# Kernel tuning notes

Hardware: AMD Instinct MI355X
Metric: run time of the kernel (lower is better)

The kernel has to match this reference:

```python
import jax, jax.numpy as jnp
import numpy as np

B, C, D = 8192, 1000, 2048
CLAMP_MIN, CLAMP_MAX = 1e-12, 1e12
SEP_WEIGHT = 0.001


def setup_inputs() -> dict:
    key = jax.random.key(0)
    k1, k2, k3 = jax.random.split(key, 3)
    x = jax.random.normal(k1, (B, D), dtype=jnp.float32)
    centers = jax.random.normal(k2, (C, D), dtype=jnp.float32)
    labels = jax.random.randint(k3, (B,), 0, C, dtype=jnp.int64)
    return {"x": x, "centers": centers, "labels": labels}


def reference(x, centers, labels):
    distmat = (
        jnp.sum(x * x, axis=1, keepdims=True)
        + jnp.sum(centers * centers, axis=1)[None, :]
        - 2.0 * (x @ centers.T)
    )
    d = jnp.clip(distmat, CLAMP_MIN, CLAMP_MAX)
    mask = labels[:, None] == jnp.arange(C, dtype=labels.dtype)[None, :]  # [B, C]
    bsz = x.shape[0]
    ncls = centers.shape[0]
    # each row has exactly one True in mask -> counts are B and B*(C-1)
    center_loss = jnp.sum(jnp.where(mask, d, 0.0)) / bsz
    sep_loss = jnp.sum(jnp.where(mask, 0.0, d)) / (bsz * (ncls - 1))
    return center_loss - SEP_WEIGHT * sep_loss
```

## Files before the change

kernel.cpp:

```cpp
#include <hip/hip_runtime.h>


#define DD 2048
#define NB 8192
#define NC 1000
#define D4 (DD / 4)
#define HALF4 256
#define THREADS 256
#define XROWS 4
#define XBLOCKS ((NB / XROWS) * 2)
#define CTILES 8
#define CRG 8
#define CBLOCKS (CTILES * CRG)

#define CQ_OFF   0
#define SC_OFF   65536
#define CSQ_OFF  73728
#define PART_OFF 73984

__device__ __forceinline__ float dot4(float4 a, float4 b) {
    return a.x * b.x + a.y * b.y + a.z * b.z + a.w * b.w;
}
__device__ __forceinline__ void acc4(float4& a, float4 b) {
    a.x += b.x; a.y += b.y; a.z += b.z; a.w += b.w;
}

__global__ __launch_bounds__(THREADS) void centers_kernel(
        const float4* __restrict__ c4, float4* __restrict__ cq,
        float* __restrict__ csq_part) {
    const int t = threadIdx.x;
    const int tile = blockIdx.x & (CTILES - 1);
    const int rg = blockIdx.x >> 3;
    const int col4 = tile * 64 + (t & 63);
    const int rlane = t >> 6;
    const int row0 = rg * 125;

    float4 acc = make_float4(0.f, 0.f, 0.f, 0.f);
    float csq = 0.f;
#pragma unroll 4
    for (int r = rlane; r < 125; r += 4) {
        float4 v = c4[(size_t)(row0 + r) * D4 + col4];
        acc4(acc, v);
        csq += dot4(v, v);
    }

    __shared__ float4 lds[4][64];
    lds[rlane][t & 63] = acc;
    __syncthreads();
    if (t < 64) {
        float4 s = lds[0][t];
        acc4(s, lds[1][t]); acc4(s, lds[2][t]); acc4(s, lds[3][t]);
        cq[rg * 512 + tile * 64 + t] = s;
    }

    __shared__ float red[THREADS / 64];
    for (int off = 32; off > 0; off >>= 1) csq += __shfl_down(csq, off, 64);
    const int lane = t & 63, wv = t >> 6;
    if (lane == 0) red[wv] = csq;
    __syncthreads();
    if (t == 0)
        csq_part[blockIdx.x] = red[0] + red[1] + red[2] + red[3];
}

__global__ __launch_bounds__(THREADS) void sc_fold_kernel(
        const float4* __restrict__ cq, float4* __restrict__ sc4) {
    const int idx = blockIdx.x * THREADS + threadIdx.x;
    float4 s = cq[idx];
#pragma unroll
    for (int r = 1; r < CRG; ++r) acc4(s, cq[r * 512 + idx]);
    sc4[idx] = s;
}

__global__ __launch_bounds__(THREADS, 8) void x_kernel(
        const float4* __restrict__ x4, const float4* __restrict__ c4,
        const int* __restrict__ labels, const float4* __restrict__ sc4,
        float4* __restrict__ partials) {
    const int t = threadIdx.x;
    const int b = blockIdx.x;
    const int rowgrp = b >> 1;
    const int h = (b & 1) * HALF4;
    const int rows0 = rowgrp * XROWS;

    const float4* xr = x4 + (size_t)rows0 * D4 + h + t;
    const float4* cbase = c4 + h + t;

    const int4 la = *(const int4*)(labels + rows0);
    const int labs[XROWS] = {la.x, la.y, la.z, la.w};

    const float4 sc = sc4[h + t];

    float4 xa = xr[0],      ca = cbase[(size_t)labs[0] * D4];
    float4 xb = xr[D4],     cb = cbase[(size_t)labs[1] * D4];

    float sx = 0.f, sdot = 0.f, scl = 0.f, s2 = 0.f;

#pragma unroll
    for (int r = 0; r < XROWS; ++r) {
        float4 nx, nc;
        if (r + 2 < XROWS) {
            nx = xr[(size_t)(r + 2) * D4];
            nc = cbase[(size_t)labs[r + 2] * D4];
        }
        sx   += dot4(xa, xa);
        sdot += dot4(xa, ca);
        scl  += dot4(ca, ca);
        s2   += dot4(xa, sc);
        xa = xb; ca = cb;
        if (r + 2 < XROWS) { xb = nx; cb = nc; }
    }

    __shared__ float red[4][THREADS / 64];
    for (int off = 32; off > 0; off >>= 1) {
        sx   += __shfl_down(sx, off, 64);
        sdot += __shfl_down(sdot, off, 64);
        scl  += __shfl_down(scl, off, 64);
        s2   += __shfl_down(s2, off, 64);
    }
    const int lane = t & 63, wv = t >> 6;
    if (lane == 0) {
        red[0][wv] = sx; red[1][wv] = sdot;
        red[2][wv] = scl; red[3][wv] = s2;
    }
    __syncthreads();
    if (t == 0) {
        float4 s;
        s.x = red[0][0] + red[0][1] + red[0][2] + red[0][3];
        s.y = red[1][0] + red[1][1] + red[1][2] + red[1][3];
        s.z = red[2][0] + red[2][1] + red[2][2] + red[2][3];
        s.w = red[3][0] + red[3][1] + red[3][2] + red[3][3];
        partials[b] = s;
    }
}

__global__ __launch_bounds__(THREADS) void finalize_kernel(
        const float4* __restrict__ partials, const float* __restrict__ csq_part,
        float* __restrict__ out) {
    const int t = threadIdx.x;

    double sx = 0.0, sdot = 0.0, scl = 0.0, s2 = 0.0, csq = 0.0;
    for (int i = t; i < XBLOCKS; i += THREADS) {
        float4 p = partials[i];
        sx += (double)p.x; sdot += (double)p.y;
        scl += (double)p.z; s2 += (double)p.w;
    }
    if (t < CBLOCKS) csq = (double)csq_part[t];

    __shared__ double red[5][THREADS / 64];
    for (int off = 32; off > 0; off >>= 1) {
        sx   += __shfl_down(sx, off, 64);
        sdot += __shfl_down(sdot, off, 64);
        scl  += __shfl_down(scl, off, 64);
        s2   += __shfl_down(s2, off, 64);
        csq  += __shfl_down(csq, off, 64);
    }
    const int lane = t & 63, wv = t >> 6;
    if (lane == 0) {
        red[0][wv] = sx; red[1][wv] = sdot; red[2][wv] = scl;
        red[3][wv] = s2; red[4][wv] = csq;
    }
    __syncthreads();
    if (t == 0) {
        double Sx   = red[0][0] + red[0][1] + red[0][2] + red[0][3];
        double Sdot = red[1][0] + red[1][1] + red[1][2] + red[1][3];
        double Scl  = red[2][0] + red[2][1] + red[2][2] + red[2][3];
        double S2   = red[3][0] + red[3][1] + red[3][2] + red[3][3];
        double Sc   = red[4][0] + red[4][1] + red[4][2] + red[4][3];
        double sum_all  = (double)NC * Sx + (double)NB * Sc - 2.0 * S2;
        double sum_diag = Sx + Scl - 2.0 * Sdot;
        double center_loss = sum_diag / (double)NB;
        double sep_loss =
            (sum_all - sum_diag) / ((double)NB * (double)(NC - 1));
        out[0] = (float)(center_loss - 0.001 * sep_loss);
    }
}

extern "C" void kernel_launch(void* const* d_in, const int* in_sizes, int n_in,
                              void* d_out, int out_size, void* d_ws, size_t ws_size,
                              hipStream_t stream) {
    const float4* x4 = (const float4*)d_in[0];
    const float4* c4 = (const float4*)d_in[1];
    const int* labels = (const int*)d_in[2];

    float4* cq = (float4*)((char*)d_ws + CQ_OFF);
    float4* sc = (float4*)((char*)d_ws + SC_OFF);
    float* csq_part = (float*)((char*)d_ws + CSQ_OFF);
    float4* partials = (float4*)((char*)d_ws + PART_OFF);
    float* out = (float*)d_out;

    centers_kernel<<<CBLOCKS, THREADS, 0, stream>>>(c4, cq, csq_part);
    sc_fold_kernel<<<2, THREADS, 0, stream>>>((const float4*)cq, sc);
    x_kernel<<<XBLOCKS, THREADS, 0, stream>>>(x4, c4, labels,
                                              (const float4*)sc, partials);
    finalize_kernel<<<1, THREADS, 0, stream>>>(partials, csq_part, out);
}
```

Baseline: 113.2 us.

## Fuse fold and finalize into last-block epilogues, double rows per block

Removes the separate sc_fold and finalize kernel launches by having the last-arriving block of centers_kernel and x_kernel, detected with an atomic counter, do the fold and the final reduction. Each x block now handles 8 rows instead of 4, halving the block count and partial count, and the occupancy hint in launch_bounds is dropped. A memset of the counters is added before the kernels, and the threadfence/atomic pattern adds some serialization at the end of each kernel.

```diff
diff --git a/kernel.cpp b/kernel.cpp
--- a/kernel.cpp
+++ b/kernel.cpp
@@ -7,7 +7,7 @@
 #define D4 (DD / 4)
 #define HALF4 256
 #define THREADS 256
-#define XROWS 4
+#define XROWS 8
 #define XBLOCKS ((NB / XROWS) * 2)
 #define CTILES 8
 #define CRG 8
@@ -17,6 +17,7 @@
 #define SC_OFF   65536
 #define CSQ_OFF  73728
 #define PART_OFF 73984
+#define CNT_OFF  106752
 
 __device__ __forceinline__ float dot4(float4 a, float4 b) {
     return a.x * b.x + a.y * b.y + a.z * b.z + a.w * b.w;
@@ -27,7 +28,8 @@
 
 __global__ __launch_bounds__(THREADS) void centers_kernel(
         const float4* __restrict__ c4, float4* __restrict__ cq,
-        float* __restrict__ csq_part) {
+        float* __restrict__ csq_part, float4* __restrict__ sc4,
+        unsigned int* __restrict__ cnt) {
     const int t = threadIdx.x;
     const int tile = blockIdx.x & (CTILES - 1);
     const int rg = blockIdx.x >> 3;
@@ -55,26 +57,32 @@
 
     __shared__ float red[THREADS / 64];
     for (int off = 32; off > 0; off >>= 1) csq += __shfl_down(csq, off, 64);
-    const int lane = t & 63, wv = t >> 6;
-    if (lane == 0) red[wv] = csq;
+    if ((t & 63) == 0) red[t >> 6] = csq;
     __syncthreads();
     if (t == 0)
         csq_part[blockIdx.x] = red[0] + red[1] + red[2] + red[3];
-}
-
-__global__ __launch_bounds__(THREADS) void sc_fold_kernel(
-        const float4* __restrict__ cq, float4* __restrict__ sc4) {
-    const int idx = blockIdx.x * THREADS + threadIdx.x;
-    float4 s = cq[idx];
+
+    __threadfence();
+    __shared__ unsigned int is_last;
+    if (t == 0)
+        is_last = (atomicAdd(&cnt[0], 1u) == CBLOCKS - 1) ? 1u : 0u;
+    __syncthreads();
+    if (is_last) {
+        __threadfence();
+        for (int idx = t; idx < 512; idx += THREADS) {
+            float4 s = cq[idx];
 #pragma unroll
-    for (int r = 1; r < CRG; ++r) acc4(s, cq[r * 512 + idx]);
-    sc4[idx] = s;
-}
-
-__global__ __launch_bounds__(THREADS, 8) void x_kernel(
+            for (int r = 1; r < CRG; ++r) acc4(s, cq[r * 512 + idx]);
+            sc4[idx] = s;
+        }
+    }
+}
+
+__global__ __launch_bounds__(THREADS) void x_kernel(
         const float4* __restrict__ x4, const float4* __restrict__ c4,
         const int* __restrict__ labels, const float4* __restrict__ sc4,
-        float4* __restrict__ partials) {
+        float4* __restrict__ partials, const float* __restrict__ csq_part,
+        unsigned int* __restrict__ cnt, float* __restrict__ out) {
     const int t = threadIdx.x;
     const int b = blockIdx.x;
     const int rowgrp = b >> 1;
@@ -84,8 +92,10 @@
     const float4* xr = x4 + (size_t)rows0 * D4 + h + t;
     const float4* cbase = c4 + h + t;
 
-    const int4 la = *(const int4*)(labels + rows0);
-    const int labs[XROWS] = {la.x, la.y, la.z, la.w};
+    const int4* l4 = (const int4*)(labels + rows0);
+    const int4 la = l4[0], lb4 = l4[1];
+    const int labs[XROWS] = {la.x, la.y, la.z, la.w,
+                             lb4.x, lb4.y, lb4.z, lb4.w};
 
     const float4 sc = sc4[h + t];
 
@@ -130,41 +140,42 @@
         s.w = red[3][0] + red[3][1] + red[3][2] + red[3][3];
         partials[b] = s;
     }
-}
-
-__global__ __launch_bounds__(THREADS) void finalize_kernel(
-        const float4* __restrict__ partials, const float* __restrict__ csq_part,
-        float* __restrict__ out) {
-    const int t = threadIdx.x;
-
-    double sx = 0.0, sdot = 0.0, scl = 0.0, s2 = 0.0, csq = 0.0;
+
+    __threadfence();
+    __shared__ unsigned int is_last;
+    if (t == 0)
+        is_last = (atomicAdd(&cnt[1], 1u) == XBLOCKS - 1) ? 1u : 0u;
+    __syncthreads();
+    if (!is_last) return;
+    __threadfence();
+
+    double dsx = 0.0, dsdot = 0.0, dscl = 0.0, ds2 = 0.0, dcsq = 0.0;
     for (int i = t; i < XBLOCKS; i += THREADS) {
         float4 p = partials[i];
-        sx += (double)p.x; sdot += (double)p.y;
-        scl += (double)p.z; s2 += (double)p.w;
-    }
-    if (t < CBLOCKS) csq = (double)csq_part[t];
-
-    __shared__ double red[5][THREADS / 64];
+        dsx += (double)p.x; dsdot += (double)p.y;
+        dscl += (double)p.z; ds2 += (double)p.w;
+    }
+    if (t < CBLOCKS) dcsq = (double)csq_part[t];
+
+    __shared__ double dred[5][THREADS / 64];
     for (int off = 32; off > 0; off >>= 1) {
-        sx   += __shfl_down(sx, off, 64);
-        sdot += __shfl_down(sdot, off, 64);
-        scl  += __shfl_down(scl, off, 64);
-        s2   += __shfl_down(s2, off, 64);
-        csq  += __shfl_down(csq, off, 64);
-    }
-    const int lane = t & 63, wv = t >> 6;
+        dsx   += __shfl_down(dsx, off, 64);
+        dsdot += __shfl_down(dsdot, off, 64);
+        dscl  += __shfl_down(dscl, off, 64);
+        ds2   += __shfl_down(ds2, off, 64);
+        dcsq  += __shfl_down(dcsq, off, 64);
+    }
     if (lane == 0) {
-        red[0][wv] = sx; red[1][wv] = sdot; red[2][wv] = scl;
-        red[3][wv] = s2; red[4][wv] = csq;
+        dred[0][wv] = dsx; dred[1][wv] = dsdot; dred[2][wv] = dscl;
+        dred[3][wv] = ds2; dred[4][wv] = dcsq;
     }
     __syncthreads();
     if (t == 0) {
-        double Sx   = red[0][0] + red[0][1] + red[0][2] + red[0][3];
-        double Sdot = red[1][0] + red[1][1] + red[1][2] + red[1][3];
-        double Scl  = red[2][0] + red[2][1] + red[2][2] + red[2][3];
-        double S2   = red[3][0] + red[3][1] + red[3][2] + red[3][3];
-        double Sc   = red[4][0] + red[4][1] + red[4][2] + red[4][3];
+        double Sx   = dred[0][0] + dred[0][1] + dred[0][2] + dred[0][3];
+        double Sdot = dred[1][0] + dred[1][1] + dred[1][2] + dred[1][3];
+        double Scl  = dred[2][0] + dred[2][1] + dred[2][2] + dred[2][3];
+        double S2   = dred[3][0] + dred[3][1] + dred[3][2] + dred[3][3];
+        double Sc   = dred[4][0] + dred[4][1] + dred[4][2] + dred[4][3];
         double sum_all  = (double)NC * Sx + (double)NB * Sc - 2.0 * S2;
         double sum_diag = Sx + Scl - 2.0 * Sdot;
         double center_loss = sum_diag / (double)NB;
@@ -185,11 +196,13 @@
     float4* sc = (float4*)((char*)d_ws + SC_OFF);
     float* csq_part = (float*)((char*)d_ws + CSQ_OFF);
     float4* partials = (float4*)((char*)d_ws + PART_OFF);
+    unsigned int* cnt = (unsigned int*)((char*)d_ws + CNT_OFF);
     float* out = (float*)d_out;
 
-    centers_kernel<<<CBLOCKS, THREADS, 0, stream>>>(c4, cq, csq_part);
-    sc_fold_kernel<<<2, THREADS, 0, stream>>>((const float4*)cq, sc);
+    hipMemsetAsync(cnt, 0, 2 * sizeof(unsigned int), stream);
+
+    centers_kernel<<<CBLOCKS, THREADS, 0, stream>>>(c4, cq, csq_part, sc, cnt);
     x_kernel<<<XBLOCKS, THREADS, 0, stream>>>(x4, c4, labels,
-                                              (const float4*)sc, partials);
-    finalize_kernel<<<1, THREADS, 0, stream>>>(partials, csq_part, out);
-}
+                                              (const float4*)sc, partials,
+                                              csq_part, cnt, out);
+}
```

Result: slower. 374.3 us (+230.6%).
